# Optimization experiments

Hardware: AMD Instinct MI355X
Metric: run time of the kernel (lower is better)

The kernel has to match this reference:

```python
import jax, jax.numpy as jnp
import numpy as np
import math

STAGE_NUM = 5
EPS = 1e-6

def _l2norm(a, axis):
    return a / (EPS + jnp.linalg.norm(a, axis=axis, keepdims=True))

def setup_inputs() -> dict:
    key = jax.random.key(0)
    k1, k2, k3, k4 = jax.random.split(key, 4)
    b, n, c, h, w, k, out_c = 4, 4, 256, 64, 64, 128, 256
    x = jax.random.normal(k1, (b, c, h, w), dtype=jnp.float32)
    querys = jax.random.normal(k2, (b * n, c, h, w), dtype=jnp.float32)
    # mu init: normal(0, sqrt(2/k)) then l2norm over channel dim
    mu0 = jax.random.normal(k3, (1, c, k), dtype=jnp.float32) * math.sqrt(2.0 / k)
    mu0 = _l2norm(mu0, axis=1)
    # conv weight: normal(0, sqrt(2/(kh*kw*out_c)))
    fan = 3 * 3 * out_c
    conv_w = jax.random.normal(k4, (out_c, 2 * c, 3, 3), dtype=jnp.float32) * math.sqrt(2.0 / fan)
    conv_b = jnp.zeros((out_c,), dtype=jnp.float32)
    return {"x": x, "querys": querys, "mu0": mu0, "conv_w": conv_w, "conv_b": conv_b, "n": n}

def reference(x, querys, mu0, conv_w, conv_b, n):
    b, c, h, w = x.shape
    k = mu0.shape[2]
    xf = x.reshape(b, c, h * w)                       # [b, c, L]
    mu = jnp.broadcast_to(mu0, (b, c, k))

    # EM iterations (torch.no_grad -> stop_gradient)
    def em_step(mu, _):
        z = jnp.einsum('bcl,bck->blk', xf, mu)        # [b, L, k]
        z = jax.nn.softmax(z, axis=2)
        z_ = z / (EPS + jnp.sum(z, axis=1, keepdims=True))
        mu = jnp.einsum('bcl,blk->bck', xf, z_)       # [b, c, k]
        mu = _l2norm(mu, axis=1)
        return mu, None
    mu, _ = jax.lax.scan(em_step, mu, None, length=STAGE_NUM)
    mu = jax.lax.stop_gradient(mu)

    org_query = querys                                 # [b*n, c, h, w]
    q = querys.reshape(b, n, c, h, w).transpose(0, 2, 1, 3, 4).reshape(b, c, n * h * w)
    q_z = jax.nn.softmax(jnp.einsum('bcl,bck->blk', q, mu), axis=2)  # [b, nL, k]
    q_z = jax.lax.stop_gradient(q_z)

    rec = jnp.einsum('bck,blk->bcl', mu, q_z)          # [b, c, n*h*w]
    rec = rec.reshape(b, c, n, h, w).transpose(0, 2, 1, 3, 4).reshape(b * n, c, h, w)

    cat = jnp.concatenate((org_query, rec), axis=1)    # [b*n, 2c, h, w]
    out = jax.lax.conv_general_dilated(
        cat, conv_w, window_strides=(1, 1), padding='SAME',
        dimension_numbers=('NCHW', 'OIHW', 'NCHW'))
    out = out + conv_b[None, :, None, None]
    return (out, mu)
```

## Files before the change

### kernel.cpp

```cpp
#include <hip/hip_runtime.h>
#include <hip/hip_bf16.h>

#define B   4
#define NN  4
#define C   256
#define HH  64
#define WW  64
#define L   4096
#define NL  16384
#define K   128
#define OC  256
#define IC2 512
#define EPSV 1e-6f
#define PW  66
#define PA  4356

typedef __hip_bfloat16 bf16;
typedef __attribute__((ext_vector_type(8))) __bf16 bf16x8;
typedef __attribute__((ext_vector_type(4))) float f32x4;

#define AS1(p) ((const __attribute__((address_space(1))) void*)(p))
#define AS3(p) ((__attribute__((address_space(3))) void*)(p))

__global__ void k_init(const float* __restrict__ mu0, float* __restrict__ mu_f,
                       bf16* __restrict__ mub) {
    int i = blockIdx.x * 256 + threadIdx.x;
    int rem = i & 32767;
    int k = rem >> 8, c = rem & 255;
    float v = mu0[c * 128 + k];
    mu_f[i] = v;
    mub[i]  = __float2bfloat16(v);
}

__global__ void k_prepx(const float* __restrict__ x, bf16* __restrict__ xb,
                        bf16* __restrict__ xt) {
    __shared__ float ld[64][65];
    int lt = blockIdx.x, ct = blockIdx.y, b = blockIdx.z;
    int t = threadIdx.x;
    #pragma unroll
    for (int i = 0; i < 16; i++) {
        int idx = t + i * 256;
        int ch = idx >> 6, xl = idx & 63;
        size_t a = ((size_t)b * C + ct * 64 + ch) * L + lt * 64 + xl;
        float v = x[a];
        ld[ch][xl] = v;
        xb[a] = __float2bfloat16(v);
    }
    __syncthreads();
    #pragma unroll
    for (int i = 0; i < 16; i++) {
        int idx = t + i * 256;
        int xl = idx >> 6, ch = idx & 63;
        xt[((size_t)b * L + lt * 64 + xl) * 256 + ct * 64 + ch] = __float2bfloat16(ld[ch][xl]);
    }
}

__global__ void k_prepq(const float* __restrict__ qy, bf16* __restrict__ P2) {
    __shared__ float ld[64][65];
    int y = blockIdx.x, ct = blockIdx.y, img = blockIdx.z;
    int t = threadIdx.x;
    #pragma unroll
    for (int i = 0; i < 16; i++) {
        int idx = t + i * 256;
        int ch = idx >> 6, xl = idx & 63;
        ld[ch][xl] = qy[((size_t)img * C + ct * 64 + ch) * L + y * WW + xl];
    }
    __syncthreads();
    #pragma unroll
    for (int i = 0; i < 16; i++) {
        int idx = t + i * 256;
        int xl = idx >> 6, ch = idx & 63;
        P2[((size_t)img * PA + (size_t)(y + 1) * PW + xl + 1) * 512 + ct * 64 + ch] =
            __float2bfloat16(ld[ch][xl]);
    }
}

__global__ void k_zborder(uint4* __restrict__ P2) {
    int pi = blockIdx.x, img = blockIdx.y, t = threadIdx.x;
    int y, x;
    if      (pi < 66)  { y = 0;        x = pi; }
    else if (pi < 132) { y = 65;       x = pi - 66; }
    else if (pi < 196) { y = pi - 131; x = 0; }
    else               { y = pi - 195; x = 65; }
    P2[((size_t)img * PA + (size_t)y * PW + x) * 64 + t] = uint4{0, 0, 0, 0};
}

__global__ void k_wprep(const float* __restrict__ cw, bf16* __restrict__ wb) {
    int idx = blockIdx.x * 256 + threadIdx.x;
    if (idx >= 9 * OC * IC2) return;
    int r  = idx / (OC * IC2);
    int oc = (idx / IC2) & 255;
    int ic = idx & 511;
    wb[idx] = __float2bfloat16(cw[((size_t)oc * IC2 + ic) * 9 + r]);
}

__global__ void __launch_bounds__(256) k_z(const bf16* __restrict__ xt,
                                           const bf16* __restrict__ mub,
                                           bf16* __restrict__ zt) {
    __shared__ __align__(16) char smem[12288];
    char* tA = smem;
    char* tB = smem + 8192;
    int t = threadIdx.x, w = t >> 6, lane = t & 63;
    int b = blockIdx.y, l0 = blockIdx.x * 64;
    const bf16* Ab = mub + (size_t)b * K * C;
    const bf16* Bb = xt + ((size_t)b * L + l0) * C;
    int srow = t >> 2, sseg = t & 3, aseg = sseg ^ (srow & 3);
    char* dA0 = tA + w * 1024;
    char* dA1 = tA + 4096 + w * 1024;
    char* dB  = tB + w * 1024;
    int aoff[8], boff;
    #pragma unroll
    for (int i = 0; i < 8; i++) {
        int rowA = i * 16 + (lane & 15);
        aoff[i] = rowA * 64 + (((lane >> 4) ^ (rowA & 3)) << 4);
    }
    { int rowB = w * 16 + (lane & 15);
      boff = rowB * 64 + (((lane >> 4) ^ (rowB & 3)) << 4); }
    f32x4 acc[8];
    #pragma unroll
    for (int i = 0; i < 8; i++) acc[i] = f32x4{0.f, 0.f, 0.f, 0.f};
    for (int s = 0; s < 8; s++) {
        int cb0 = s * 32 + aseg * 8;
        __syncthreads();
        __builtin_amdgcn_global_load_lds(AS1(Ab + (size_t)srow * C + cb0),        AS3(dA0), 16, 0, 0);
        __builtin_amdgcn_global_load_lds(AS1(Ab + (size_t)(srow + 64) * C + cb0), AS3(dA1), 16, 0, 0);
        __builtin_amdgcn_global_load_lds(AS1(Bb + (size_t)srow * C + cb0),        AS3(dB),  16, 0, 0);
        __syncthreads();
        bf16x8 bfr = *(bf16x8*)(tB + boff);
        #pragma unroll
        for (int i = 0; i < 8; i++) {
            bf16x8 af = *(bf16x8*)(tA + aoff[i]);
            acc[i] = __builtin_amdgcn_mfma_f32_16x16x32_bf16(af, bfr, acc[i], 0, 0, 0);
        }
    }
    float m = -1e30f;
    #pragma unroll
    for (int i = 0; i < 8; i++)
        #pragma unroll
        for (int r = 0; r < 4; r++) m = fmaxf(m, acc[i][r]);
    m = fmaxf(m, __shfl_xor(m, 16, 64));
    m = fmaxf(m, __shfl_xor(m, 32, 64));
    float ssum = 0.f;
    #pragma unroll
    for (int i = 0; i < 8; i++)
        #pragma unroll
        for (int r = 0; r < 4; r++) { acc[i][r] = __expf(acc[i][r] - m); ssum += acc[i][r]; }
    ssum += __shfl_xor(ssum, 16, 64);
    ssum += __shfl_xor(ssum, 32, 64);
    float inv = 1.f / ssum;
    int quad = lane >> 4, col = lane & 15;
    bf16* zb = zt + (size_t)b * K * L + l0 + w * 16 + col;
    #pragma unroll
    for (int i = 0; i < 8; i++)
        #pragma unroll
        for (int r = 0; r < 4; r++) {
            int k = i * 16 + quad * 4 + r;
            zb[(size_t)k * L] = __float2bfloat16(acc[i][r] * inv);
        }
}

__global__ void __launch_bounds__(256) k_mu(const bf16* __restrict__ zt,
                                            const bf16* __restrict__ xb,
                                            float* __restrict__ part) {
    __shared__ __align__(16) char smem[12288];
    char* tA = smem;
    char* tB = smem + 8192;
    int t = threadIdx.x, w = t >> 6, lane = t & 63;
    int ct = blockIdx.x, chunk = blockIdx.y, b = blockIdx.z;
    const bf16* Ab = zt + (size_t)b * K * L + chunk * 256;
    const bf16* Bb = xb + ((size_t)b * C + ct * 64) * L + chunk * 256;
    int srow = t >> 2, sseg = t & 3, aseg = sseg ^ (srow & 3);
    char* dA0 = tA + w * 1024; char* dA1 = tA + 4096 + w * 1024;
    char* dB0 = tB + w * 1024;
    int wm = w >> 1, wn = w & 1;
    int aoff[4], boff[2];
    #pragma unroll
    for (int i = 0; i < 4; i++) {
        int rowA = wm * 64 + i * 16 + (lane & 15);
        aoff[i] = rowA * 64 + (((lane >> 4) ^ (rowA & 3)) << 4);
    }
    #pragma unroll
    for (int j = 0; j < 2; j++) {
        int rowB = wn * 32 + j * 16 + (lane & 15);
        boff[j] = rowB * 64 + (((lane >> 4) ^ (rowB & 3)) << 4);
    }
    f32x4 acc[4][2];
    #pragma unroll
    for (int i = 0; i < 4; i++)
        #pragma unroll
        for (int j = 0; j < 2; j++) acc[i][j] = f32x4{0.f, 0.f, 0.f, 0.f};
    for (int s = 0; s < 8; s++) {
        int lb = s * 32 + aseg * 8;
        __syncthreads();
        __builtin_amdgcn_global_load_lds(AS1(Ab + (size_t)srow * L + lb),        AS3(dA0), 16, 0, 0);
        __builtin_amdgcn_global_load_lds(AS1(Ab + (size_t)(srow + 64) * L + lb), AS3(dA1), 16, 0, 0);
        __builtin_amdgcn_global_load_lds(AS1(Bb + (size_t)srow * L + lb),        AS3(dB0), 16, 0, 0);
        __syncthreads();
        bf16x8 af[4], bfr[2];
        #pragma unroll
        for (int i = 0; i < 4; i++) af[i]  = *(bf16x8*)(tA + aoff[i]);
        #pragma unroll
        for (int j = 0; j < 2; j++) bfr[j] = *(bf16x8*)(tB + boff[j]);
        #pragma unroll
        for (int i = 0; i < 4; i++)
            #pragma unroll
            for (int j = 0; j < 2; j++)
                acc[i][j] = __builtin_amdgcn_mfma_f32_16x16x32_bf16(af[i], bfr[j], acc[i][j], 0, 0, 0);
    }
    float* pb = part + ((size_t)(b * 16 + chunk) * K) * C + ct * 64;
    int quad = lane >> 4, col = lane & 15;
    #pragma unroll
    for (int i = 0; i < 4; i++) {
        int k = wm * 64 + i * 16 + quad * 4;
        #pragma unroll
        for (int j = 0; j < 2; j++) {
            int c = wn * 32 + j * 16 + col;
            #pragma unroll
            for (int r = 0; r < 4; r++)
                pb[(size_t)(k + r) * C + c] = acc[i][j][r];
        }
    }
}

__global__ void k_norm(const float* __restrict__ part, float* __restrict__ mu_f,
                       bf16* __restrict__ mub, bf16* __restrict__ muT) {
    int b = blockIdx.x >> 7, k = blockIdx.x & 127, lane = threadIdx.x;
    float v[4] = {0.f, 0.f, 0.f, 0.f};
    for (int ch = 0; ch < 16; ch++) {
        const float* p = part + ((size_t)(b * 16 + ch) * K + k) * C;
        #pragma unroll
        for (int j = 0; j < 4; j++) v[j] += p[lane + j * 64];
    }
    float s = v[0]*v[0] + v[1]*v[1] + v[2]*v[2] + v[3]*v[3];
    for (int o = 32; o > 0; o >>= 1) s += __shfl_xor(s, o, 64);
    float r = 1.f / (EPSV + sqrtf(s));
    float* mf = mu_f + ((size_t)b * K + k) * C;
    bf16*  mb = mub  + ((size_t)b * K + k) * C;
    bf16*  mt = muT  + (size_t)b * C * K + k;
    #pragma unroll
    for (int j = 0; j < 4; j++) {
        float val = v[j] * r;
        int c = lane + j * 64;
        mf[c] = val;
        mb[c] = __float2bfloat16(val);
        mt[(size_t)c * K] = __float2bfloat16(val);
    }
}

__global__ void __launch_bounds__(256) k_qz(const bf16* __restrict__ P2,
                                            const bf16* __restrict__ mub,
                                            bf16* __restrict__ qz) {
    __shared__ __align__(16) char smem[12288];
    char* tA = smem;
    char* tB = smem + 4096;
    int t = threadIdx.x, w = t >> 6, lane = t & 63;
    int b = blockIdx.y, tile = blockIdx.x;
    int n = tile >> 6, y = tile & 63;
    int img = b * NN + n;
    const bf16* Ab = P2 + ((size_t)img * PA + (size_t)(y + 1) * PW + 1) * 512;
    const bf16* Bb = mub + (size_t)b * K * C;
    int srow = t >> 2, sseg = t & 3, aseg = sseg ^ (srow & 3);
    char* dA  = tA + w * 1024;
    char* dB0 = tB + w * 1024;
    char* dB1 = tB + 4096 + w * 1024;
    int boff[8], aoff;
    #pragma unroll
    for (int j = 0; j < 8; j++) {
        int rowB = j * 16 + (lane & 15);
        boff[j] = rowB * 64 + (((lane >> 4) ^ (rowB & 3)) << 4);
    }
    { int rowA = w * 16 + (lane & 15);
      aoff = rowA * 64 + (((lane >> 4) ^ (rowA & 3)) << 4); }
    f32x4 acc[8];
    #pragma unroll
    for (int j = 0; j < 8; j++) acc[j] = f32x4{0.f, 0.f, 0.f, 0.f};
    for (int s = 0; s < 8; s++) {
        int cb0 = s * 32 + aseg * 8;
        __syncthreads();
        __builtin_amdgcn_global_load_lds(AS1(Ab + (size_t)srow * 512 + cb0),      AS3(dA),  16, 0, 0);
        __builtin_amdgcn_global_load_lds(AS1(Bb + (size_t)srow * C + cb0),        AS3(dB0), 16, 0, 0);
        __builtin_amdgcn_global_load_lds(AS1(Bb + (size_t)(srow + 64) * C + cb0), AS3(dB1), 16, 0, 0);
        __syncthreads();
        bf16x8 af = *(bf16x8*)(tA + aoff);
        #pragma unroll
        for (int j = 0; j < 8; j++) {
            bf16x8 bfr = *(bf16x8*)(tB + boff[j]);
            acc[j] = __builtin_amdgcn_mfma_f32_16x16x32_bf16(af, bfr, acc[j], 0, 0, 0);
        }
    }
    int quad = lane >> 4, col = lane & 15;
    bf16* qb = qz + ((size_t)b * NL + n * L + y * WW + w * 16 + quad * 4) * K;
    #pragma unroll
    for (int r = 0; r < 4; r++) {
        float mm = acc[0][r];
        #pragma unroll
        for (int j = 1; j < 8; j++) mm = fmaxf(mm, acc[j][r]);
        mm = fmaxf(mm, __shfl_xor(mm, 1, 64));
        mm = fmaxf(mm, __shfl_xor(mm, 2, 64));
        mm = fmaxf(mm, __shfl_xor(mm, 4, 64));
        mm = fmaxf(mm, __shfl_xor(mm, 8, 64));
        float ss = 0.f;
        float e[8];
        #pragma unroll
        for (int j = 0; j < 8; j++) { e[j] = __expf(acc[j][r] - mm); ss += e[j]; }
        ss += __shfl_xor(ss, 1, 64);
        ss += __shfl_xor(ss, 2, 64);
        ss += __shfl_xor(ss, 4, 64);
        ss += __shfl_xor(ss, 8, 64);
        float inv = 1.f / ss;
        #pragma unroll
        for (int j = 0; j < 8; j++)
            qb[(size_t)r * K + j * 16 + col] = __float2bfloat16(e[j] * inv);
    }
}

__global__ void __launch_bounds__(256) k_rec(const bf16* __restrict__ qz,
                                             const bf16* __restrict__ muT,
                                             bf16* __restrict__ P2) {
    __shared__ __align__(16) char smem[16384];
    char* tA = smem; char* tB = smem + 8192;
    int t = threadIdx.x, w = t >> 6, lane = t & 63;
    int ct = blockIdx.x, lt = blockIdx.y, b = blockIdx.z;
    const bf16* Ab = qz + ((size_t)b * NL + lt * 128) * K;
    const bf16* Bb = muT + ((size_t)b * C + ct * 128) * K;
    int srow = t >> 2, sseg = t & 3, aseg = sseg ^ (srow & 3);
    char* dA0 = tA + w * 1024; char* dA1 = tA + 4096 + w * 1024;
    char* dB0 = tB + w * 1024; char* dB1 = tB + 4096 + w * 1024;
    int wm = w >> 1, wn = w & 1;
    int aoff[4], boff[4];
    #pragma unroll
    for (int i = 0; i < 4; i++) {
        int rowA = wm * 64 + i * 16 + (lane & 15);
        aoff[i] = rowA * 64 + (((lane >> 4) ^ (rowA & 3)) << 4);
        int rowB = wn * 64 + i * 16 + (lane & 15);
        boff[i] = rowB * 64 + (((lane >> 4) ^ (rowB & 3)) << 4);
    }
    f32x4 acc[4][4];
    #pragma unroll
    for (int i = 0; i < 4; i++)
        #pragma unroll
        for (int j = 0; j < 4; j++) acc[i][j] = f32x4{0.f, 0.f, 0.f, 0.f};
    for (int s = 0; s < 4; s++) {
        int kb = s * 32 + aseg * 8;
        __syncthreads();
        __builtin_amdgcn_global_load_lds(AS1(Ab + (size_t)srow * K + kb),        AS3(dA0), 16, 0, 0);
        __builtin_amdgcn_global_load_lds(AS1(Ab + (size_t)(srow + 64) * K + kb), AS3(dA1), 16, 0, 0);
        __builtin_amdgcn_global_load_lds(AS1(Bb + (size_t)srow * K + kb),        AS3(dB0), 16, 0, 0);
        __builtin_amdgcn_global_load_lds(AS1(Bb + (size_t)(srow + 64) * K + kb), AS3(dB1), 16, 0, 0);
        __syncthreads();
        bf16x8 af[4], bfr[4];
        #pragma unroll
        for (int i = 0; i < 4; i++) af[i]  = *(bf16x8*)(tA + aoff[i]);
        #pragma unroll
        for (int j = 0; j < 4; j++) bfr[j] = *(bf16x8*)(tB + boff[j]);
        #pragma unroll
        for (int i = 0; i < 4; i++)
            #pragma unroll
            for (int j = 0; j < 4; j++)
                acc[i][j] = __builtin_amdgcn_mfma_f32_16x16x32_bf16(af[i], bfr[j], acc[i][j], 0, 0, 0);
    }
    int quad = lane >> 4, col = lane & 15;
    #pragma unroll
    for (int i = 0; i < 4; i++) {
        int lbase = lt * 128 + wm * 64 + i * 16 + quad * 4;
        #pragma unroll
        for (int r = 0; r < 4; r++) {
            int l = lbase + r;
            int n = l >> 12, p = l & 4095;
            int y = p >> 6, xp = p & 63;
            bf16* dst = P2 + ((size_t)(b * NN + n) * PA + (size_t)(y + 1) * PW + xp + 1) * 512 + 256;
            #pragma unroll
            for (int j = 0; j < 4; j++)
                dst[ct * 128 + wn * 64 + j * 16 + col] = __float2bfloat16(acc[i][j][r]);
        }
    }
}

__global__ void __launch_bounds__(256, 2) k_conv(const bf16* __restrict__ P2,
                                                 const bf16* __restrict__ Wb,
                                                 const float* __restrict__ cb,
                                                 float* __restrict__ out) {
    __shared__ __align__(16) char smem[49920];
    char* inl = smem;
    char* wld = smem + 25344;
    int t = threadIdx.x, w = t >> 6, lane = t & 63;
    int m0  = blockIdx.x * 128;
    int y0  = blockIdx.y * 4;
    int img = blockIdx.z;
    int srow = t >> 2;
    int aseg = (t & 3) ^ ((srow ^ (srow >> 2)) & 3);
    int wm = w >> 1, wn = w & 1;
    int q = lane >> 4, lane15 = lane & 15;

    int aoff[4];
    #pragma unroll
    for (int i = 0; i < 4; i++) {
        int rowA = wm * 64 + i * 16 + lane15;
        aoff[i] = rowA * 64 + (((q ^ (rowA ^ (rowA >> 2))) & 3) << 4);
    }

    auto stageIN = [&](int cc) {
        size_t ibase = (size_t)img * PA * 512 + cc * 32;
        #pragma unroll
        for (int it = 0; it < 6; it++) {
            unsigned g = it * 256 + t;
            unsigned row = g / 264u, ps = g - row * 264u;
            unsigned px = ps >> 2, s0 = ps & 3;
            unsigned sg = s0 ^ ((px ^ (px >> 1)) & 3);
            __builtin_amdgcn_global_load_lds(
                AS1(P2 + ibase + ((size_t)(y0 + row) * PW + px) * 512 + sg * 8),
                AS3(inl + it * 4096 + w * 1024), 16, 0, 0);
        }
        if (t < 48) {
            unsigned g = 1536 + t;
            unsigned row = g / 264u, ps = g - row * 264u;
            unsigned px = ps >> 2, s0 = ps & 3;
            unsigned sg = s0 ^ ((px ^ (px >> 1)) & 3);
            __builtin_amdgcn_global_load_lds(
                AS1(P2 + ibase + ((size_t)(y0 + row) * PW + px) * 512 + sg * 8),
                AS3(inl + 24576), 16, 0, 0);
        }
    };

    f32x4 acc[4][8];
    #pragma unroll
    for (int i = 0; i < 4; i++) {
        int oc = m0 + wm * 64 + i * 16 + q * 4;
        #pragma unroll
        for (int r = 0; r < 4; r++) {
            float bv = cb[oc + r];
            #pragma unroll
            for (int j = 0; j < 8; j++) acc[i][j][r] = bv;
        }
    }

    stageIN(0);
    {
        const bf16* w0 = Wb + (size_t)(m0 + srow) * IC2 + aseg * 8;
        __builtin_amdgcn_global_load_lds(AS1(w0),                         AS3(wld + w * 1024), 16, 0, 0);
        __builtin_amdgcn_global_load_lds(AS1(w0 + (size_t)64 * IC2),      AS3(wld + 4096 + w * 1024), 16, 0, 0);
        const bf16* w1 = w0 + (size_t)(OC * IC2);
        __builtin_amdgcn_global_load_lds(AS1(w1),                         AS3(wld + 8192 + w * 1024), 16, 0, 0);
        __builtin_amdgcn_global_load_lds(AS1(w1 + (size_t)64 * IC2),      AS3(wld + 8192 + 4096 + w * 1024), 16, 0, 0);
    }
    asm volatile("s_waitcnt vmcnt(0)" ::: "memory");
    __builtin_amdgcn_s_barrier();
    asm volatile("" ::: "memory");

    for (int cc = 0; cc < 16; cc++) {
        #pragma unroll
        for (int rt = 0; rt < 9; rt++) {
            const int dy = rt / 3, dx = rt % 3;
            char* wbuf = wld + (rt % 3) * 8192;
            bf16x8 af[4];
            #pragma unroll
            for (int i = 0; i < 4; i++) af[i] = *(bf16x8*)(wbuf + aoff[i]);
            const bool doPf = (cc * 9 + rt + 2) < 144;
            if (doPf) {
                const int g2 = rt + 2;
                const int rt2 = (g2 >= 9) ? g2 - 9 : g2;
                const int cc2 = cc + (g2 >= 9 ? 1 : 0);
                char* wdst = wld + ((rt + 2) % 3) * 8192;
                const bf16* wsrc = Wb + (size_t)rt2 * (OC * IC2) + (size_t)(m0 + srow) * IC2
                                 + cc2 * 32 + aseg * 8;
                __builtin_amdgcn_global_load_lds(AS1(wsrc),                    AS3(wdst + w * 1024), 16, 0, 0);
                __builtin_amdgcn_global_load_lds(AS1(wsrc + (size_t)64 * IC2), AS3(wdst + 4096 + w * 1024), 16, 0, 0);
            }
            __builtin_amdgcn_s_setprio(1);
            #pragma unroll
            for (int j = 0; j < 8; j++) {
                int p = (j & 3) * 16 + lane15 + dx;
                int rowsel = 2 * wn + (j >> 2) + dy;
                bf16x8 bfr = *(bf16x8*)(inl + rowsel * 4224 + p * 64 +
                                        (((q ^ (p ^ (p >> 1))) & 3) << 4));
                #pragma unroll
                for (int i = 0; i < 4; i++)
                    acc[i][j] = __builtin_amdgcn_mfma_f32_16x16x32_bf16(af[i], bfr, acc[i][j], 0, 0, 0);
            }
            __builtin_amdgcn_s_setprio(0);
            if (rt == 8) {
                if (cc < 15) {
                    asm volatile("" ::: "memory");
                    __builtin_amdgcn_s_barrier();
                    asm volatile("" ::: "memory");
                    stageIN(cc + 1);
                    asm volatile("s_waitcnt vmcnt(0)" ::: "memory");
                    __builtin_amdgcn_s_barrier();
                    asm volatile("" ::: "memory");
                }
            } else {
                if (doPf) asm volatile("s_waitcnt vmcnt(2)" ::: "memory");
                else      asm volatile("s_waitcnt vmcnt(0)" ::: "memory");
                __builtin_amdgcn_s_barrier();
                asm volatile("" ::: "memory");
            }
        }
    }

    #pragma unroll
    for (int i = 0; i < 4; i++) {
        int oc = m0 + wm * 64 + i * 16 + q * 4;
        #pragma unroll
        for (int j = 0; j < 8; j++) {
            int px = blockIdx.y * 256 + wn * 128 + (j >> 2) * 64 + (j & 3) * 16 + lane15;
            #pragma unroll
            for (int r = 0; r < 4; r++)
                out[((size_t)img * OC + oc + r) * L + px] = acc[i][j][r];
        }
    }
}

__global__ void k_muout(const float* __restrict__ mu_f, float* __restrict__ out) {
    int i = blockIdx.x * 256 + threadIdx.x;
    int b = i >> 15, rem = i & 32767;
    int c = rem >> 7, k = rem & 127;
    out[(size_t)16777216 + i] = mu_f[((size_t)b * K + k) * C + c];
}

extern "C" void kernel_launch(void* const* d_in, const int* in_sizes, int n_in,
                              void* d_out, int out_size, void* d_ws, size_t ws_size,
                              hipStream_t stream) {
    const float* x   = (const float*)d_in[0];
    const float* qy  = (const float*)d_in[1];
    const float* mu0 = (const float*)d_in[2];
    const float* cw  = (const float*)d_in[3];
    const float* cb  = (const float*)d_in[4];
    float* out = (float*)d_out;

    char* ws = (char*)d_ws;
    float* mu_f = (float*)(ws);
    bf16*  mu_b = (bf16*) (ws + 524288);
    bf16*  muT  = (bf16*) (ws + 786432);
    bf16*  Wb   = (bf16*) (ws + 1048576);
    bf16*  zt   = (bf16*) (ws + 3407872);
    bf16*  qz   = (bf16*) (ws + 3407872);
    bf16*  P2   = (bf16*) (ws + 20185088);
    bf16*  x_bf = (bf16*) (ws + 20185088);
    float* part = (float*)(ws + 20185088 + 8388608);
    bf16*  xt   = (bf16*) (ws + 20185088 + 16777216);

    k_init<<<512, 256, 0, stream>>>(mu0, mu_f, mu_b);
    k_prepx<<<dim3(64, 4, 4), 256, 0, stream>>>(x, x_bf, xt);

    for (int it = 0; it < 5; it++) {
        k_z<<<dim3(64, 4), 256, 0, stream>>>(xt, mu_b, zt);
        k_mu<<<dim3(4, 16, 4), 256, 0, stream>>>(zt, x_bf, part);
        k_norm<<<512, 64, 0, stream>>>(part, mu_f, mu_b, muT);
    }

    k_prepq<<<dim3(64, 4, 16), 256, 0, stream>>>(qy, P2);
    k_zborder<<<dim3(260, 16), 64, 0, stream>>>((uint4*)P2);
    k_wprep<<<4608, 256, 0, stream>>>(cw, Wb);

    k_qz<<<dim3(256, 4), 256, 0, stream>>>(P2, mu_b, qz);
    k_rec<<<dim3(2, 128, 4), 256, 0, stream>>>(qz, muT, P2);
    k_conv<<<dim3(2, 16, 16), 256, 0, stream>>>(P2, Wb, cb, out);
    k_muout<<<512, 256, 0, stream>>>(mu_f, out);
}
```

Before: 400.1 us.

## Fuse query softmax and reconstruction GEMM into one kernel via LDS

Merges k_qz and k_rec into one kernel. The softmax probabilities for a 64-pixel row tile stay in shared memory, and the block then multiplies them by muT to write the reconstructed channels straight into the padded P2 buffer. This removes the qz round trip through global memory and one launch. In exchange, LDS per block rises to about 45KB, which lowers occupancy, and each block reloads all of muT serially, with two barriers per stage.

```diff
diff --git a/kernel.cpp b/kernel.cpp
--- a/kernel.cpp
+++ b/kernel.cpp
@@ -247,30 +247,34 @@
     }
 }
 
-__global__ void __launch_bounds__(256) k_qz(const bf16* __restrict__ P2,
-                                            const bf16* __restrict__ mub,
-                                            bf16* __restrict__ qz) {
-    __shared__ __align__(16) char smem[12288];
+__global__ void __launch_bounds__(256) k_qzrec(const bf16* __restrict__ P2r,
+                                               const bf16* __restrict__ mub,
+                                               const bf16* __restrict__ muT,
+                                               bf16* __restrict__ P2w) {
+    __shared__ __align__(16) char smem[46080];
     char* tA = smem;
     char* tB = smem + 4096;
+    char* zl = smem + 12288;
+    char* mt = smem + 29696;
     int t = threadIdx.x, w = t >> 6, lane = t & 63;
     int b = blockIdx.y, tile = blockIdx.x;
     int n = tile >> 6, y = tile & 63;
     int img = b * NN + n;
-    const bf16* Ab = P2 + ((size_t)img * PA + (size_t)(y + 1) * PW + 1) * 512;
+    const bf16* Ab = P2r + ((size_t)img * PA + (size_t)(y + 1) * PW + 1) * 512;
     const bf16* Bb = mub + (size_t)b * K * C;
     int srow = t >> 2, sseg = t & 3, aseg = sseg ^ (srow & 3);
     char* dA  = tA + w * 1024;
     char* dB0 = tB + w * 1024;
     char* dB1 = tB + 4096 + w * 1024;
+    int q = lane >> 4, col = lane & 15;
     int boff[8], aoff;
     #pragma unroll
     for (int j = 0; j < 8; j++) {
-        int rowB = j * 16 + (lane & 15);
-        boff[j] = rowB * 64 + (((lane >> 4) ^ (rowB & 3)) << 4);
-    }
-    { int rowA = w * 16 + (lane & 15);
-      aoff = rowA * 64 + (((lane >> 4) ^ (rowA & 3)) << 4); }
+        int rowB = j * 16 + col;
+        boff[j] = rowB * 64 + ((q ^ (rowB & 3)) << 4);
+    }
+    { int rowA = w * 16 + col;
+      aoff = rowA * 64 + ((q ^ (rowA & 3)) << 4); }
     f32x4 acc[8];
     #pragma unroll
     for (int j = 0; j < 8; j++) acc[j] = f32x4{0.f, 0.f, 0.f, 0.f};
@@ -288,8 +292,6 @@
             acc[j] = __builtin_amdgcn_mfma_f32_16x16x32_bf16(af, bfr, acc[j], 0, 0, 0);
         }
     }
-    int quad = lane >> 4, col = lane & 15;
-    bf16* qb = qz + ((size_t)b * NL + n * L + y * WW + w * 16 + quad * 4) * K;
     #pragma unroll
     for (int r = 0; r < 4; r++) {
         float mm = acc[0][r];
@@ -308,71 +310,55 @@
         ss += __shfl_xor(ss, 4, 64);
         ss += __shfl_xor(ss, 8, 64);
         float inv = 1.f / ss;
+        int zrow = w * 16 + q * 4 + r;
         #pragma unroll
         for (int j = 0; j < 8; j++)
-            qb[(size_t)r * K + j * 16 + col] = __float2bfloat16(e[j] * inv);
-    }
-}
-
-__global__ void __launch_bounds__(256) k_rec(const bf16* __restrict__ qz,
-                                             const bf16* __restrict__ muT,
-                                             bf16* __restrict__ P2) {
-    __shared__ __align__(16) char smem[16384];
-    char* tA = smem; char* tB = smem + 8192;
-    int t = threadIdx.x, w = t >> 6, lane = t & 63;
-    int ct = blockIdx.x, lt = blockIdx.y, b = blockIdx.z;
-    const bf16* Ab = qz + ((size_t)b * NL + lt * 128) * K;
-    const bf16* Bb = muT + ((size_t)b * C + ct * 128) * K;
-    int srow = t >> 2, sseg = t & 3, aseg = sseg ^ (srow & 3);
-    char* dA0 = tA + w * 1024; char* dA1 = tA + 4096 + w * 1024;
-    char* dB0 = tB + w * 1024; char* dB1 = tB + 4096 + w * 1024;
-    int wm = w >> 1, wn = w & 1;
-    int aoff[4], boff[4];
-    #pragma unroll
-    for (int i = 0; i < 4; i++) {
-        int rowA = wm * 64 + i * 16 + (lane & 15);
-        aoff[i] = rowA * 64 + (((lane >> 4) ^ (rowA & 3)) << 4);
-        int rowB = wn * 64 + i * 16 + (lane & 15);
-        boff[i] = rowB * 64 + (((lane >> 4) ^ (rowB & 3)) << 4);
-    }
-    f32x4 acc[4][4];
-    #pragma unroll
-    for (int i = 0; i < 4; i++)
-        #pragma unroll
-        for (int j = 0; j < 4; j++) acc[i][j] = f32x4{0.f, 0.f, 0.f, 0.f};
+            *(bf16*)(zl + zrow * 272 + (j * 16 + col) * 2) = __float2bfloat16(e[j] * inv);
+    }
+    const bf16* Mb = muT + (size_t)b * C * K;
+    int mrow = (lane >> 2);
+    int mseg = lane & 3;
+    #pragma unroll
+    for (int it2 = 0; it2 < 4; it2++) {
+        int row = w * 64 + it2 * 16 + mrow;
+        int sg = mseg ^ ((row ^ (row >> 2)) & 3);
+        __builtin_amdgcn_global_load_lds(AS1(Mb + (size_t)row * K + sg * 8),
+            AS3(mt + (w * 64 + it2 * 16) * 64), 16, 0, 0);
+    }
+    __syncthreads();
+    bf16x8 afz[4];
+    #pragma unroll
+    for (int ch = 0; ch < 4; ch++)
+        afz[ch] = *(bf16x8*)(zl + (w * 16 + col) * 272 + ch * 64 + q * 16);
+    f32x4 acc2[16];
+    #pragma unroll
+    for (int j = 0; j < 16; j++) acc2[j] = f32x4{0.f, 0.f, 0.f, 0.f};
     for (int s = 0; s < 4; s++) {
-        int kb = s * 32 + aseg * 8;
-        __syncthreads();
-        __builtin_amdgcn_global_load_lds(AS1(Ab + (size_t)srow * K + kb),        AS3(dA0), 16, 0, 0);
-        __builtin_amdgcn_global_load_lds(AS1(Ab + (size_t)(srow + 64) * K + kb), AS3(dA1), 16, 0, 0);
-        __builtin_amdgcn_global_load_lds(AS1(Bb + (size_t)srow * K + kb),        AS3(dB0), 16, 0, 0);
-        __builtin_amdgcn_global_load_lds(AS1(Bb + (size_t)(srow + 64) * K + kb), AS3(dB1), 16, 0, 0);
-        __syncthreads();
-        bf16x8 af[4], bfr[4];
-        #pragma unroll
-        for (int i = 0; i < 4; i++) af[i]  = *(bf16x8*)(tA + aoff[i]);
-        #pragma unroll
-        for (int j = 0; j < 4; j++) bfr[j] = *(bf16x8*)(tB + boff[j]);
-        #pragma unroll
-        for (int i = 0; i < 4; i++)
-            #pragma unroll
-            for (int j = 0; j < 4; j++)
-                acc[i][j] = __builtin_amdgcn_mfma_f32_16x16x32_bf16(af[i], bfr[j], acc[i][j], 0, 0, 0);
-    }
-    int quad = lane >> 4, col = lane & 15;
-    #pragma unroll
-    for (int i = 0; i < 4; i++) {
-        int lbase = lt * 128 + wm * 64 + i * 16 + quad * 4;
-        #pragma unroll
-        for (int r = 0; r < 4; r++) {
-            int l = lbase + r;
-            int n = l >> 12, p = l & 4095;
-            int y = p >> 6, xp = p & 63;
-            bf16* dst = P2 + ((size_t)(b * NN + n) * PA + (size_t)(y + 1) * PW + xp + 1) * 512 + 256;
-            #pragma unroll
-            for (int j = 0; j < 4; j++)
-                dst[ct * 128 + wn * 64 + j * 16 + col] = __float2bfloat16(acc[i][j][r]);
-        }
+        #pragma unroll
+        for (int j = 0; j < 16; j++) {
+            int rr = j * 16 + col;
+            bf16x8 bm = *(bf16x8*)(mt + rr * 64 + ((q ^ ((rr ^ (rr >> 2)) & 3)) << 4));
+            acc2[j] = __builtin_amdgcn_mfma_f32_16x16x32_bf16(afz[s], bm, acc2[j], 0, 0, 0);
+        }
+        if (s < 3) {
+            __syncthreads();
+            #pragma unroll
+            for (int it2 = 0; it2 < 4; it2++) {
+                int row = w * 64 + it2 * 16 + mrow;
+                int sg = mseg ^ ((row ^ (row >> 2)) & 3);
+                __builtin_amdgcn_global_load_lds(AS1(Mb + (size_t)row * K + (s + 1) * 32 + sg * 8),
+                    AS3(mt + (w * 64 + it2 * 16) * 64), 16, 0, 0);
+            }
+            __syncthreads();
+        }
+    }
+    #pragma unroll
+    for (int r = 0; r < 4; r++) {
+        int xg = w * 16 + q * 4 + r;
+        bf16* dst = P2w + ((size_t)img * PA + (size_t)(y + 1) * PW + xg + 1) * 512 + 256;
+        #pragma unroll
+        for (int j = 0; j < 16; j++)
+            dst[j * 16 + col] = __float2bfloat16(acc2[j][r]);
     }
 }
 
@@ -533,7 +519,6 @@
     bf16*  muT  = (bf16*) (ws + 786432);
     bf16*  Wb   = (bf16*) (ws + 1048576);
     bf16*  zt   = (bf16*) (ws + 3407872);
-    bf16*  qz   = (bf16*) (ws + 3407872);
     bf16*  P2   = (bf16*) (ws + 20185088);
     bf16*  x_bf = (bf16*) (ws + 20185088);
     float* part = (float*)(ws + 20185088 + 8388608);
@@ -552,8 +537,7 @@
     k_zborder<<<dim3(260, 16), 64, 0, stream>>>((uint4*)P2);
     k_wprep<<<4608, 256, 0, stream>>>(cw, Wb);
 
-    k_qz<<<dim3(256, 4), 256, 0, stream>>>(P2, mu_b, qz);
-    k_rec<<<dim3(2, 128, 4), 256, 0, stream>>>(qz, muT, P2);
+    k_qzrec<<<dim3(256, 4), 256, 0, stream>>>(P2, mu_b, muT, P2);
     k_conv<<<dim3(2, 16, 16), 256, 0, stream>>>(P2, Wb, cb, out);
     k_muout<<<512, 256, 0, stream>>>(mu_f, out);
 }
```

Result: no change. 405.3 us (+1.3%).
